# Optimization experiments

Hardware: AMD Instinct MI355X
Metric: run time of the kernel (lower is better)

Reference implementation:

```python
import jax, jax.numpy as jnp
import numpy as np

BASE_P = 0.99
MIN_P = 0.9


def setup_inputs() -> dict:
    key = jax.random.key(0)
    k1, k2, k3 = jax.random.split(key, 3)
    B, T, C = 32, 4096, 256
    return {
        "student_latents": jax.random.normal(k1, (B, T, C), dtype=jnp.float32),
        "teacher_latents": jax.random.normal(k2, (B, T, C), dtype=jnp.float32),
        "risk_coef": jax.random.uniform(k3, (B,), dtype=jnp.float32),
    }


def reference(student_latents, teacher_latents, risk_coef):
    # 1) Epistemic uncertainty: per-token MSE between student and teacher  [B, T]
    delta = jnp.mean((student_latents - teacher_latents) ** 2, axis=-1)
    uncertainty = jnp.clip(delta * 2.0, 0.0, 1.0)
    # 2) Distrust = max(U, risk * U)  [B, T]
    distrust = jnp.maximum(uncertainty, risk_coef[:, None] * uncertainty)
    # 3) Dynamic percentile per sample  [B]
    distrust_b = jnp.mean(distrust, axis=1)
    p_eff = BASE_P - (BASE_P - MIN_P) * distrust_b
    # 4) Per-sample quantile threshold of |x| over flattened (T*C), then clamp.
    B = student_latents.shape[0]
    s = jnp.abs(student_latents).reshape(B, -1).astype(jnp.float32)
    # torch detaches before quantile -> no gradient through the threshold
    thresh = jax.lax.stop_gradient(
        jax.vmap(lambda a, q: jnp.quantile(a, q))(s, p_eff.astype(jnp.float32))
    )  # [B], linear interpolation matches torch.quantile default
    t = thresh[:, None, None].astype(student_latents.dtype)
    return jnp.clip(student_latents, -t, t)
```

## Files before the change

### kernel.cpp

```cpp
#include <hip/hip_runtime.h>
#include <stdint.h>

#define B_ 32
#define T_ 4096
#define C_ 256
#define N_ (T_*C_)
#define NB 8192

#define HIST_BYTES (B_*NB*4)
#define USUM_OFF   (HIST_BYTES)
#define THR_OFF    (USUM_OFF + 128)

typedef float f32x4 __attribute__((ext_vector_type(4)));

__global__ __launch_bounds__(512, 8) void k1_uncert_hist(
    const float* __restrict__ s, const float* __restrict__ t,
    float* __restrict__ usum, unsigned* __restrict__ ghist)
{
    __shared__ unsigned lhist[4096];
    __shared__ float part[64*65];
    __shared__ float wu[8];
    const int tid = threadIdx.x;
    #pragma unroll
    for (int k = tid; k < 4096; k += 512) lhist[k] = 0;
    __syncthreads();

    const int b = blockIdx.x >> 6;
    const size_t base4 = (size_t)blockIdx.x * 4096;
    const f32x4* s4 = (const f32x4*)s + base4;
    const f32x4* t4 = (const f32x4*)t + base4;
    const int lane = tid & 63, wid = tid >> 6;

    int i = wid*128 + lane;
    f32x4 a0 = s4[i];
    f32x4 a1 = s4[i + 64];
    f32x4 c0 = __builtin_nontemporal_load(t4 + i);
    f32x4 c1 = __builtin_nontemporal_load(t4 + i + 64);

    #pragma unroll
    for (int it = 0; it < 4; ++it) {
        f32x4 b0, b1, d0, d1;
        const int inext = i + 1024;
        if (it < 3) {
            b0 = s4[inext];
            b1 = s4[inext + 64];
            d0 = __builtin_nontemporal_load(t4 + inext);
            d1 = __builtin_nontemporal_load(t4 + inext + 64);
        }

        float dx = a0.x-c0.x, dy = a0.y-c0.y, dz = a0.z-c0.z, dw = a0.w-c0.w;
        float sum0 = dx*dx + dy*dy + dz*dz + dw*dw;
        float ex = a1.x-c1.x, ey = a1.y-c1.y, ez = a1.z-c1.z, ew = a1.w-c1.w;
        float sum1 = ex*ex + ey*ey + ez*ez + ew*ew;

        {
            unsigned u;
            u = __float_as_uint(a0.x); atomicAdd(&lhist[(u>>19)&0xFFF], 1u << (((u>>18)&1u)<<4));
            u = __float_as_uint(a0.y); atomicAdd(&lhist[(u>>19)&0xFFF], 1u << (((u>>18)&1u)<<4));
            u = __float_as_uint(a0.z); atomicAdd(&lhist[(u>>19)&0xFFF], 1u << (((u>>18)&1u)<<4));
            u = __float_as_uint(a0.w); atomicAdd(&lhist[(u>>19)&0xFFF], 1u << (((u>>18)&1u)<<4));
            u = __float_as_uint(a1.x); atomicAdd(&lhist[(u>>19)&0xFFF], 1u << (((u>>18)&1u)<<4));
            u = __float_as_uint(a1.y); atomicAdd(&lhist[(u>>19)&0xFFF], 1u << (((u>>18)&1u)<<4));
            u = __float_as_uint(a1.z); atomicAdd(&lhist[(u>>19)&0xFFF], 1u << (((u>>18)&1u)<<4));
            u = __float_as_uint(a1.w); atomicAdd(&lhist[(u>>19)&0xFFF], 1u << (((u>>18)&1u)<<4));
        }

        const int tk = it*16 + wid*2;
        part[tk*65 + lane]     = sum0;
        part[(tk+1)*65 + lane] = sum1;

        if (it < 3) { a0 = b0; a1 = b1; c0 = d0; c1 = d1; }
        i = inext;
    }
    __syncthreads();

    {
        const int tok = tid >> 3, q = tid & 7;
        const float* pp = &part[tok*65 + q*8];
        float ps = pp[0]+pp[1]+pp[2]+pp[3]+pp[4]+pp[5]+pp[6]+pp[7];
        ps += __shfl_xor(ps, 1, 64);
        ps += __shfl_xor(ps, 2, 64);
        ps += __shfl_xor(ps, 4, 64);
        float u = fminf(ps * (1.0f/128.0f), 1.0f);
        u += __shfl_xor(u, 8, 64);
        u += __shfl_xor(u, 16, 64);
        u += __shfl_xor(u, 32, 64);
        if (lane == 0) wu[wid] = u;
    }
    __syncthreads();
    if (tid == 0) {
        float a = 0.f;
        #pragma unroll
        for (int w = 0; w < 8; ++w) a += wu[w];
        atomicAdd(&usum[b], a);
    }

    unsigned* gh = ghist + (size_t)b * NB;
    #pragma unroll
    for (int w = tid; w < 4096; w += 512) {
        const unsigned pc = lhist[w];
        if (pc) {
            const unsigned lo = pc & 0xFFFFu, hi = pc >> 16;
            if (lo) atomicAdd(&gh[2*w],   lo);
            if (hi) atomicAdd(&gh[2*w+1], hi);
        }
    }
}

__global__ __launch_bounds__(256) void k2_thresh(
    const unsigned* __restrict__ ghist, const float* __restrict__ usum,
    const float* __restrict__ risk, float* __restrict__ thr)
{
    __shared__ unsigned lh[NB];
    __shared__ unsigned sc[256];
    __shared__ float res[2];
    const int b = blockIdx.x, tid = threadIdx.x;
    const unsigned* gh = ghist + (size_t)b * NB;
    for (int j = tid; j < NB; j += 256) lh[j] = gh[j];
    __syncthreads();

    unsigned p = 0;
    #pragma unroll
    for (int k = 0; k < 32; ++k) p += lh[tid*32 + k];
    sc[tid] = p;
    __syncthreads();
    #pragma unroll
    for (int d = 1; d < 256; d <<= 1) {
        unsigned v = (tid >= d) ? sc[tid - d] : 0u;
        __syncthreads();
        sc[tid] += v;
        __syncthreads();
    }
    const unsigned incl = sc[tid];
    const unsigned excl = incl - p;

    const float distrust = usum[b] * fmaxf(1.f, risk[b]) * (1.0f/(float)T_);
    const double pq  = 0.99 - 0.09 * (double)distrust;
    const double pos = pq * (double)(N_ - 1);
    const unsigned i0 = (unsigned)pos;
    const float g = (float)(pos - (double)i0);

    #pragma unroll
    for (int r = 0; r < 2; ++r) {
        const unsigned rk = i0 + (unsigned)r;
        if (excl <= rk && rk < incl) {
            unsigned cum = excl, cnt = 1;
            int bin = tid*32 + 31;
            #pragma unroll
            for (int k = 0; k < 32; ++k) {
                const unsigned c = lh[tid*32 + k];
                if (cum + c > rk) { bin = tid*32 + k; cnt = c; break; }
                cum += c;
            }
            const float lo = __uint_as_float((unsigned)bin << 18);
            const float hi = __uint_as_float((unsigned)(bin + 1) << 18);
            const unsigned j = rk - cum;
            res[r] = lo + ((float)(j + 1) / (float)(cnt + 1)) * (hi - lo);
        }
    }
    __syncthreads();
    if (tid == 0) thr[b] = res[0] + g * (res[1] - res[0]);
}

__global__ __launch_bounds__(256) void k3_clip(
    const float* __restrict__ s, const float* __restrict__ thr,
    float* __restrict__ out)
{
    const int bid = blockIdx.x;
    const int b = bid >> 7;
    const float t = thr[b];
    const size_t base = (size_t)bid * 2048 + threadIdx.x;
    const f32x4* s4 = (const f32x4*)s;
    f32x4* o4 = (f32x4*)out;

    f32x4 v[8];
    #pragma unroll
    for (int k = 0; k < 8; ++k) v[k] = s4[base + (size_t)k*256];
    #pragma unroll
    for (int k = 0; k < 8; ++k) {
        f32x4 a = v[k];
        a.x = fminf(fmaxf(a.x, -t), t);
        a.y = fminf(fmaxf(a.y, -t), t);
        a.z = fminf(fmaxf(a.z, -t), t);
        a.w = fminf(fmaxf(a.w, -t), t);
        __builtin_nontemporal_store(a, o4 + base + (size_t)k*256);
    }
}

extern "C" void kernel_launch(void* const* d_in, const int* in_sizes, int n_in,
                              void* d_out, int out_size, void* d_ws, size_t ws_size,
                              hipStream_t stream) {
    const float* s    = (const float*)d_in[0];
    const float* t    = (const float*)d_in[1];
    const float* risk = (const float*)d_in[2];
    float* out = (float*)d_out;
    char* ws = (char*)d_ws;

    unsigned* hist = (unsigned*)(ws);
    float*    usum = (float*)(ws + USUM_OFF);
    float*    thr  = (float*)(ws + THR_OFF);

    hipMemsetAsync(ws, 0, HIST_BYTES + 256, stream);

    k1_uncert_hist<<<2048, 512, 0, stream>>>(s, t, usum, hist);
    k2_thresh<<<B_, 256, 0, stream>>>(hist, usum, risk, thr);
    k3_clip<<<4096, 256, 0, stream>>>(s, thr, out);
}
```

Before: 338.3 us.

## Deepen load prefetch, flush histogram earlier, replace usum atomics with per-block partials

The first kernel now issues three to four tile loads up front before the histogram and MSE work, so more global memory traffic is in flight per thread. The global histogram flush moves to right after the first barrier, and the per-token partial buffer is padded to allow vectorized float4 LDS reads. Per-block uncertainty sums are written to a partial array and reduced in the threshold kernel instead of using float atomics, which also makes that sum deterministic. The deeper prefetch raises register pressure and could lower occupancy under the 512x8 launch bound.

```diff
diff --git a/kernel.cpp b/kernel.cpp
--- a/kernel.cpp
+++ b/kernel.cpp
@@ -8,17 +8,17 @@
 #define NB 8192
 
 #define HIST_BYTES (B_*NB*4)
-#define USUM_OFF   (HIST_BYTES)
-#define THR_OFF    (USUM_OFF + 128)
+#define UPART_OFF  (HIST_BYTES)
+#define THR_OFF    (UPART_OFF + 2048*4)
 
 typedef float f32x4 __attribute__((ext_vector_type(4)));
 
 __global__ __launch_bounds__(512, 8) void k1_uncert_hist(
     const float* __restrict__ s, const float* __restrict__ t,
-    float* __restrict__ usum, unsigned* __restrict__ ghist)
+    float* __restrict__ upart, unsigned* __restrict__ ghist)
 {
     __shared__ unsigned lhist[4096];
-    __shared__ float part[64*65];
+    __shared__ float part[64*68];
     __shared__ float wu[8];
     const int tid = threadIdx.x;
     #pragma unroll
@@ -30,54 +30,60 @@
     const f32x4* s4 = (const f32x4*)s + base4;
     const f32x4* t4 = (const f32x4*)t + base4;
     const int lane = tid & 63, wid = tid >> 6;
-
-    int i = wid*128 + lane;
-    f32x4 a0 = s4[i];
-    f32x4 a1 = s4[i + 64];
-    f32x4 c0 = __builtin_nontemporal_load(t4 + i);
-    f32x4 c1 = __builtin_nontemporal_load(t4 + i + 64);
-
-    #pragma unroll
-    for (int it = 0; it < 4; ++it) {
-        f32x4 b0, b1, d0, d1;
-        const int inext = i + 1024;
-        if (it < 3) {
-            b0 = s4[inext];
-            b1 = s4[inext + 64];
-            d0 = __builtin_nontemporal_load(t4 + inext);
-            d1 = __builtin_nontemporal_load(t4 + inext + 64);
+    const int v0 = wid*128 + lane;
+
+#define LOADT(n, OFF) \
+    f32x4 sa##n = s4[v0 + (OFF)]; \
+    f32x4 sb##n = s4[v0 + (OFF) + 64]; \
+    f32x4 ta##n = __builtin_nontemporal_load(t4 + v0 + (OFF)); \
+    f32x4 tb##n = __builtin_nontemporal_load(t4 + v0 + (OFF) + 64);
+
+#define HIST1(x) { unsigned u = __float_as_uint(x); \
+    atomicAdd(&lhist[(u>>19)&0xFFFu], 1u << (((u>>18)&1u)<<4)); }
+
+#define COMP(n, IT) { \
+    HIST1(sa##n.x) HIST1(sa##n.y) HIST1(sa##n.z) HIST1(sa##n.w) \
+    HIST1(sb##n.x) HIST1(sb##n.y) HIST1(sb##n.z) HIST1(sb##n.w) \
+    float dx = sa##n.x-ta##n.x, dy = sa##n.y-ta##n.y, \
+          dz = sa##n.z-ta##n.z, dw = sa##n.w-ta##n.w; \
+    float sum0 = dx*dx + dy*dy + dz*dz + dw*dw; \
+    float ex = sb##n.x-tb##n.x, ey = sb##n.y-tb##n.y, \
+          ez = sb##n.z-tb##n.z, ew = sb##n.w-tb##n.w; \
+    float sum1 = ex*ex + ey*ey + ez*ez + ew*ew; \
+    const int tk = (IT)*16 + wid*2; \
+    part[tk*68 + lane]     = sum0; \
+    part[(tk+1)*68 + lane] = sum1; }
+
+    LOADT(0, 0)
+    LOADT(1, 1024)
+    LOADT(2, 2048)
+    COMP(0, 0)
+    LOADT(3, 3072)
+    COMP(1, 1)
+    COMP(2, 2)
+    COMP(3, 3)
+#undef LOADT
+#undef HIST1
+#undef COMP
+
+    __syncthreads();
+
+    unsigned* gh = ghist + (size_t)b * NB;
+    #pragma unroll
+    for (int w = tid; w < 4096; w += 512) {
+        const unsigned pc = lhist[w];
+        if (pc) {
+            const unsigned lo = pc & 0xFFFFu, hi = pc >> 16;
+            if (lo) atomicAdd(&gh[2*w],   lo);
+            if (hi) atomicAdd(&gh[2*w+1], hi);
         }
-
-        float dx = a0.x-c0.x, dy = a0.y-c0.y, dz = a0.z-c0.z, dw = a0.w-c0.w;
-        float sum0 = dx*dx + dy*dy + dz*dz + dw*dw;
-        float ex = a1.x-c1.x, ey = a1.y-c1.y, ez = a1.z-c1.z, ew = a1.w-c1.w;
-        float sum1 = ex*ex + ey*ey + ez*ez + ew*ew;
-
-        {
-            unsigned u;
-            u = __float_as_uint(a0.x); atomicAdd(&lhist[(u>>19)&0xFFF], 1u << (((u>>18)&1u)<<4));
-            u = __float_as_uint(a0.y); atomicAdd(&lhist[(u>>19)&0xFFF], 1u << (((u>>18)&1u)<<4));
-            u = __float_as_uint(a0.z); atomicAdd(&lhist[(u>>19)&0xFFF], 1u << (((u>>18)&1u)<<4));
-            u = __float_as_uint(a0.w); atomicAdd(&lhist[(u>>19)&0xFFF], 1u << (((u>>18)&1u)<<4));
-            u = __float_as_uint(a1.x); atomicAdd(&lhist[(u>>19)&0xFFF], 1u << (((u>>18)&1u)<<4));
-            u = __float_as_uint(a1.y); atomicAdd(&lhist[(u>>19)&0xFFF], 1u << (((u>>18)&1u)<<4));
-            u = __float_as_uint(a1.z); atomicAdd(&lhist[(u>>19)&0xFFF], 1u << (((u>>18)&1u)<<4));
-            u = __float_as_uint(a1.w); atomicAdd(&lhist[(u>>19)&0xFFF], 1u << (((u>>18)&1u)<<4));
-        }
-
-        const int tk = it*16 + wid*2;
-        part[tk*65 + lane]     = sum0;
-        part[(tk+1)*65 + lane] = sum1;
-
-        if (it < 3) { a0 = b0; a1 = b1; c0 = d0; c1 = d1; }
-        i = inext;
-    }
-    __syncthreads();
+    }
 
     {
         const int tok = tid >> 3, q = tid & 7;
-        const float* pp = &part[tok*65 + q*8];
-        float ps = pp[0]+pp[1]+pp[2]+pp[3]+pp[4]+pp[5]+pp[6]+pp[7];
+        const f32x4* pp = (const f32x4*)&part[tok*68 + q*8];
+        f32x4 r0 = pp[0], r1 = pp[1];
+        float ps = r0.x+r0.y+r0.z+r0.w + r1.x+r1.y+r1.z+r1.w;
         ps += __shfl_xor(ps, 1, 64);
         ps += __shfl_xor(ps, 2, 64);
         ps += __shfl_xor(ps, 4, 64);
@@ -92,31 +98,31 @@
         float a = 0.f;
         #pragma unroll
         for (int w = 0; w < 8; ++w) a += wu[w];
-        atomicAdd(&usum[b], a);
-    }
-
-    unsigned* gh = ghist + (size_t)b * NB;
-    #pragma unroll
-    for (int w = tid; w < 4096; w += 512) {
-        const unsigned pc = lhist[w];
-        if (pc) {
-            const unsigned lo = pc & 0xFFFFu, hi = pc >> 16;
-            if (lo) atomicAdd(&gh[2*w],   lo);
-            if (hi) atomicAdd(&gh[2*w+1], hi);
-        }
+        upart[blockIdx.x] = a;
     }
 }
 
 __global__ __launch_bounds__(256) void k2_thresh(
-    const unsigned* __restrict__ ghist, const float* __restrict__ usum,
+    const unsigned* __restrict__ ghist, const float* __restrict__ upart,
     const float* __restrict__ risk, float* __restrict__ thr)
 {
     __shared__ unsigned lh[NB];
     __shared__ unsigned sc[256];
     __shared__ float res[2];
+    __shared__ float susum;
     const int b = blockIdx.x, tid = threadIdx.x;
     const unsigned* gh = ghist + (size_t)b * NB;
     for (int j = tid; j < NB; j += 256) lh[j] = gh[j];
+    if (tid < 64) {
+        float v = upart[b*64 + tid];
+        v += __shfl_xor(v, 1, 64);
+        v += __shfl_xor(v, 2, 64);
+        v += __shfl_xor(v, 4, 64);
+        v += __shfl_xor(v, 8, 64);
+        v += __shfl_xor(v, 16, 64);
+        v += __shfl_xor(v, 32, 64);
+        if (tid == 0) susum = v;
+    }
     __syncthreads();
 
     unsigned p = 0;
@@ -134,7 +140,7 @@
     const unsigned incl = sc[tid];
     const unsigned excl = incl - p;
 
-    const float distrust = usum[b] * fmaxf(1.f, risk[b]) * (1.0f/(float)T_);
+    const float distrust = susum * fmaxf(1.f, risk[b]) * (1.0f/(float)T_);
     const double pq  = 0.99 - 0.09 * (double)distrust;
     const double pos = pq * (double)(N_ - 1);
     const unsigned i0 = (unsigned)pos;
@@ -196,13 +202,13 @@
     float* out = (float*)d_out;
     char* ws = (char*)d_ws;
 
-    unsigned* hist = (unsigned*)(ws);
-    float*    usum = (float*)(ws + USUM_OFF);
-    float*    thr  = (float*)(ws + THR_OFF);
-
-    hipMemsetAsync(ws, 0, HIST_BYTES + 256, stream);
-
-    k1_uncert_hist<<<2048, 512, 0, stream>>>(s, t, usum, hist);
-    k2_thresh<<<B_, 256, 0, stream>>>(hist, usum, risk, thr);
+    unsigned* hist  = (unsigned*)(ws);
+    float*    upart = (float*)(ws + UPART_OFF);
+    float*    thr   = (float*)(ws + THR_OFF);
+
+    hipMemsetAsync(ws, 0, HIST_BYTES, stream);
+
+    k1_uncert_hist<<<2048, 512, 0, stream>>>(s, t, upart, hist);
+    k2_thresh<<<B_, 256, 0, stream>>>(hist, upart, risk, thr);
     k3_clip<<<4096, 256, 0, stream>>>(s, thr, out);
 }
```

Result: no change. 343.0 us (+1.4%).
